# Optimization experiments

Measured on AMD Instinct MI355X. Metric: run time of the kernel, lower is better.

The kernel has to match this reference:

```python
import jax, jax.numpy as jnp
import numpy as np

B, LSEQ = 128, 4096
NUM_EXPERTS, TOP_K = 8, 2
OUT_SEQ = 256
AUX_FACTOR = 0.01


def _conv1d(x, w, b, stride, pad):
    # x: [B, Cin, L], w: [Cout, Cin, K]
    y = jax.lax.conv_general_dilated(x, w, (stride,), [(pad, pad)],
                                     dimension_numbers=('NCH', 'OIH', 'NCH'))
    return y + b[None, :, None]


def setup_inputs() -> dict:
    key = jax.random.key(0)
    ks = jax.random.split(key, 9)
    s = 0.05
    return {
        'x': jax.random.normal(ks[0], (B, LSEQ), jnp.float32),
        # gating conv net (in_channels=2 -> 32 -> 64, kernel 5, padding same)
        'g_w1': jax.random.normal(ks[1], (32, 2, 5), jnp.float32) * s,
        'g_b1': jnp.zeros((32,), jnp.float32),
        'g_w2': jax.random.normal(ks[2], (64, 32, 5), jnp.float32) * s,
        'g_b2': jnp.zeros((64,), jnp.float32),
        # gating MLP (64 -> 128 -> num_experts)
        'm_w1': jax.random.normal(ks[3], (128, 64), jnp.float32) * s,
        'm_b1': jnp.zeros((128,), jnp.float32),
        'm_w2': jax.random.normal(ks[4], (NUM_EXPERTS, 128), jnp.float32) * s,
        'm_b2': jnp.zeros((NUM_EXPERTS,), jnp.float32),
        # expert CNN stacks, stacked over experts (same shapes per expert)
        'ew1': jax.random.normal(ks[5], (NUM_EXPERTS, 64, 2, 7), jnp.float32) * s,
        'eb1': jnp.zeros((NUM_EXPERTS, 64), jnp.float32),
        'ew2': jax.random.normal(ks[6], (NUM_EXPERTS, 128, 64, 5), jnp.float32) * s,
        'eb2': jnp.zeros((NUM_EXPERTS, 128), jnp.float32),
        'ew3': jax.random.normal(ks[7], (NUM_EXPERTS, 128, 128, 3), jnp.float32) * s,
        'eb3': jnp.zeros((NUM_EXPERTS, 128), jnp.float32),
    }


def reference(x, g_w1, g_b1, g_w2, g_b2, m_w1, m_b1, m_w2, m_b2,
              ew1, eb1, ew2, eb2, ew3, eb3):
    b, lseq = x.shape
    # periodic Hann window (torch.hann_window default)
    win = 0.5 * (1.0 - jnp.cos(2.0 * jnp.pi * jnp.arange(lseq, dtype=x.dtype) / lseq))
    xf = jnp.fft.rfft(x * win, norm='ortho')
    fft = jnp.stack([xf.real, xf.imag], axis=1)  # [B, 2, Lf]

    # gating: conv -> relu -> conv -> relu -> global avg pool -> MLP (dropout in eval)
    h = jax.nn.relu(_conv1d(fft, g_w1, g_b1, 1, 2))
    h = jax.nn.relu(_conv1d(h, g_w2, g_b2, 1, 2))
    pooled = h.mean(-1)  # [B, 64]
    logits = jax.nn.relu(pooled @ m_w1.T + m_b1) @ m_w2.T + m_b2  # [B, E]
    rw = jax.nn.softmax(logits, axis=1)
    aux = AUX_FACTOR * NUM_EXPERTS * (rw.mean(0) * logits.mean(0)).sum()

    tw, ti = jax.lax.top_k(rw, TOP_K)  # [B, K]
    tw = tw / tw.sum(-1, keepdims=True)

    # Each (token, k) pair routes fft[b] to expert ti[b,k]; compute each expert
    # densely over the batch and gather (same math as masked dispatch/combine).
    def expert(w1, b1, w2, b2, w3, b3):
        e = jax.nn.relu(_conv1d(fft, w1, b1, 2, 3))
        e = jax.nn.relu(_conv1d(e, w2, b2, 2, 2))
        e = jax.nn.relu(_conv1d(e, w3, b3, 1, 1))
        return e

    out_stack = jax.vmap(expert)(ew1, eb1, ew2, eb2, ew3, eb3)  # [E, B, C, L]
    sel = out_stack[ti, jnp.arange(b)[:, None]]                 # [B, K, C, L]
    final = (sel * tw[:, :, None, None]).sum(1)                 # [B, C, L]

    # adaptive max pool 1d to OUT_SEQ (PyTorch window rule)
    L = final.shape[-1]
    starts = np.floor(np.arange(OUT_SEQ) * L / OUT_SEQ).astype(np.int32)
    ends = np.ceil((np.arange(OUT_SEQ) + 1) * L / OUT_SEQ).astype(np.int32)
    maxw = int((ends - starts).max())
    raw = starts[:, None] + np.arange(maxw)[None, :]
    valid = jnp.asarray(raw < ends[:, None])
    idx = np.minimum(raw, L - 1)
    g = final[..., idx]  # [B, C, OUT_SEQ, maxw]
    resized = jnp.max(jnp.where(valid, g, -jnp.inf), axis=-1)
    return (resized, aux)
```

## Files before the change

### kernel.cpp

```cpp
#include <hip/hip_runtime.h>

#define NFREQ 2049
#define L1LEN 1025
#define L1STRIDE 1026
#define L2LEN 513

typedef short v8s  __attribute__((ext_vector_type(8)));
typedef float v16f __attribute__((ext_vector_type(16)));
typedef unsigned short ushort_t;
typedef unsigned int uint_t;

#define OFF_FFT     0ull
#define OFF_TWID    524544ull
#define OFF_PTW     526592ull
#define OFF_WIN     530944ull
#define OFF_PART    535040ull
#define OFF_TW      1075712ull
#define OFF_TI      1075968ull
#define OFF_SRWLOG  1076224ull
#define OFF_W2HF    1076480ull
#define OFF_W2LF    1081600ull
#define OFF_W2F     1086720ull
#define OFF_W3F     1250560ull
#define OFF_A       1447168ull
#define OFF_E2U     9852160ull

#define E1U_K_STRIDE 8404992
#define E2U_K_STRIDE 8404992

__device__ __forceinline__ float relu_f(float x) { return fmaxf(x, 0.0f); }
__device__ __forceinline__ int   rfl_i(int v)   { return __builtin_amdgcn_readfirstlane(v); }
__device__ __forceinline__ float rfl_f(float v) { return __uint_as_float((unsigned)__builtin_amdgcn_readfirstlane((int)__float_as_uint(v))); }
__device__ __forceinline__ ushort_t f2bf(float x) {
    unsigned u = __float_as_uint(x);
    unsigned r = (u + 0x7FFFu + ((u >> 16) & 1u)) >> 16;
    return (ushort_t)r;
}
__device__ __forceinline__ float bf2f(ushort_t h) { return __uint_as_float(((unsigned)h) << 16); }

__global__ void init_kernel(float* SRWLOG, float* TWID, float* PTW, float* WIN,
                            ushort_t* W2HF, ushort_t* W2LF, ushort_t* W2F, ushort_t* W3F,
                            const float* g_w2, const float* ew2, const float* ew3) {
    const float PI = 3.14159265358979323846f;
    int tid = blockIdx.x * blockDim.x + threadIdx.x;
    int stride = gridDim.x * blockDim.x;
    for (int i = tid; i < 16; i += stride) SRWLOG[i] = 0.0f;
    for (int j = tid; j < 1024; j += stride) {
        float a = PI * (float)j / 1024.0f;
        TWID[2 * j] = cosf(a);
        TWID[2 * j + 1] = -sinf(a);
    }
    for (int k = tid; k < 2049; k += stride) {
        float a = PI * (float)k / 2048.0f;
        PTW[2 * k] = cosf(a);
        PTW[2 * k + 1] = sinf(a);
    }
    for (int n = tid; n < 4096; n += stride) {
        WIN[n] = 0.5f * (1.0f - cosf(2.0f * PI * (float)n / 4096.0f));
    }
    for (int i = tid; i < 10240; i += stride) {
        int j = i & 7;
        int lane = (i >> 3) & 63;
        int ks = (i >> 9) & 1;
        int tile = (i >> 10) & 1;
        int t = i >> 11;
        int o = tile * 32 + (lane & 31);
        int c = ks * 16 + (lane >> 5) * 8 + j;
        float w = g_w2[o * 160 + c * 5 + t];
        ushort_t h = f2bf(w);
        W2HF[i] = h;
        W2LF[i] = f2bf(w - bf2f(h));
    }
    for (int i = tid; i < 327680; i += stride) {
        int j = i & 7;
        int lane = (i >> 3) & 63;
        int ks = (i >> 9) & 3;
        int w = (i >> 11) & 3;
        int t = (i >> 13) % 5;
        int e = i / 40960;
        int o = w * 32 + (lane & 31);
        int c = ks * 16 + (lane >> 5) * 8 + j;
        W2F[i] = f2bf(ew2[((e * 128 + o) * 64 + c) * 5 + t]);
    }
    for (int i = tid; i < 393216; i += stride) {
        int j = i & 7;
        int lane = (i >> 3) & 63;
        int ks = (i >> 9) & 7;
        int w = (i >> 12) & 3;
        int t = (i >> 14) % 3;
        int e = i / 49152;
        int o = w * 32 + (lane & 31);
        int c = ks * 16 + (lane >> 5) * 8 + j;
        W3F[i] = f2bf(ew3[((e * 128 + o) * 128 + c) * 3 + t]);
    }
}

__global__ __launch_bounds__(1024) void fft_kernel(const float* __restrict__ x,
                                                   const float* __restrict__ TWID,
                                                   const float* __restrict__ PTW,
                                                   const float* __restrict__ WIN,
                                                   float* __restrict__ FFT) {
    __shared__ float re[2048];
    __shared__ float im[2048];
    int b = blockIdx.x, t = threadIdx.x;
    const float* xb = x + b * 4096;
    for (int i = t; i < 2048; i += 1024) {
        int j = (int)(__brev((unsigned)i) >> 21);
        re[i] = xb[2 * j] * WIN[2 * j];
        im[i] = xb[2 * j + 1] * WIN[2 * j + 1];
    }
    for (int s = 1; s <= 11; ++s) {
        __syncthreads();
        int half = 1 << (s - 1);
        int shift = 11 - s;
        int bf = t;
        {
            int grp = bf >> (s - 1);
            int pos = bf & (half - 1);
            int i1 = (grp << s) + pos;
            int i2 = i1 + half;
            int j = pos << shift;
            float wr = TWID[2 * j], wi = TWID[2 * j + 1];
            float ar = re[i2], ai = im[i2];
            float tr = wr * ar - wi * ai;
            float ti = wr * ai + wi * ar;
            float br = re[i1], bi = im[i1];
            re[i2] = br - tr; im[i2] = bi - ti;
            re[i1] = br + tr; im[i1] = bi + ti;
        }
    }
    __syncthreads();
    const float scale = 1.0f / 64.0f;
    for (int k = t; k <= 2048; k += 1024) {
        int k1 = k & 2047;
        int k2 = (2048 - k) & 2047;
        float zr = re[k1], zi = im[k1];
        float yr = re[k2], yi = im[k2];
        float Er = 0.5f * (zr + yr), Ei = 0.5f * (zi - yi);
        float Or = 0.5f * (zi + yi), Oi = 0.5f * (yr - zr);
        float c2 = PTW[2 * k], s3 = PTW[2 * k + 1];
        FFT[b * 4098 + k]        = (Er + c2 * Or + s3 * Oi) * scale;
        FFT[b * 4098 + 2049 + k] = (Ei + c2 * Oi - s3 * Or) * scale;
    }
}

__global__ __launch_bounds__(256) void g12_kernel(const float* __restrict__ FFT,
                                                  const float* __restrict__ g_w1, const float* __restrict__ g_b1,
                                                  const ushort_t* __restrict__ W2HF, const ushort_t* __restrict__ W2LF,
                                                  const float* __restrict__ g_b2,
                                                  float* __restrict__ PART) {
    __shared__ float fx[2][72];
    __shared__ float w1S[320];
    __shared__ float b1S[32];
    __shared__ __align__(16) char un[17408];
    ushort_t (*xh)[40] = (ushort_t (*)[40])un;
    ushort_t (*xl)[40] = (ushort_t (*)[40])(un + 5440);
    float (*red)[68]  = (float (*)[68])un;
    int b = blockIdx.y;
    int q0 = blockIdx.x * 64;
    int t = threadIdx.x;
    for (int i = t; i < 352; i += 256) {
        if (i < 320) w1S[i] = g_w1[i];
        else b1S[i - 320] = g_b1[i - 320];
    }
    {
        const float* fb = FFT + b * 4098;
        for (int i = t; i < 144; i += 256) {
            int ch = i / 72, u = i % 72;
            int P = q0 - 4 + u;
            fx[ch][u] = (P >= 0 && P < NFREQ) ? fb[ch * NFREQ + P] : 0.0f;
        }
    }
    __syncthreads();
    {
        int c = t & 31;
        float bias = b1S[c];
        float wr[10];
        #pragma unroll
        for (int j = 0; j < 10; ++j) wr[j] = w1S[c * 10 + j];
        for (int i = t; i < 544; i += 256) {
            int g4 = (i >> 5) << 2;
            float4 x00 = *(const float4*)&fx[0][g4];
            float4 x01 = *(const float4*)&fx[0][g4 + 4];
            float4 x10 = *(const float4*)&fx[1][g4];
            float4 x11 = *(const float4*)&fx[1][g4 + 4];
            float xa[8] = {x00.x, x00.y, x00.z, x00.w, x01.x, x01.y, x01.z, x01.w};
            float xb_[8] = {x10.x, x10.y, x10.z, x10.w, x11.x, x11.y, x11.z, x11.w};
            #pragma unroll
            for (int rr = 0; rr < 4; ++rr) {
                int row = g4 + rr;
                int pos = q0 - 2 + row;
                ushort_t h = 0, l = 0;
                if (pos >= 0 && pos < NFREQ) {
                    float a = bias;
                    #pragma unroll
                    for (int tt = 0; tt < 5; ++tt) a = fmaf(xa[rr + tt], wr[tt], a);
                    #pragma unroll
                    for (int tt = 0; tt < 5; ++tt) a = fmaf(xb_[rr + tt], wr[5 + tt], a);
                    a = relu_f(a);
                    h = f2bf(a);
                    l = f2bf(a - bf2f(h));
                }
                xh[row][c] = h;
                xl[row][c] = l;
            }
        }
    }
    __syncthreads();
    int lane = t & 63;
    int w = rfl_i(t >> 6);
    int tile = w & 1;
    int qh = w >> 1;
    int n = lane & 31;
    int kg = lane >> 5;
    v16f acc;
    #pragma unroll
    for (int i = 0; i < 16; ++i) acc[i] = 0.0f;
    #pragma unroll
    for (int t5 = 0; t5 < 5; ++t5) {
        int row = qh * 32 + n + t5;
        #pragma unroll
        for (int ks = 0; ks < 2; ++ks) {
            int c0 = ks * 16 + kg * 8;
            v8s Ah = *(const v8s*)(W2HF + (((t5 * 2 + tile) * 2 + ks) << 9) + lane * 8);
            v8s Al = *(const v8s*)(W2LF + (((t5 * 2 + tile) * 2 + ks) << 9) + lane * 8);
            v8s Bh = *(const v8s*)&xh[row][c0];
            v8s Bl = *(const v8s*)&xl[row][c0];
            acc = __builtin_amdgcn_mfma_f32_32x32x16_bf16(Ah, Bh, acc, 0, 0, 0);
            acc = __builtin_amdgcn_mfma_f32_32x32x16_bf16(Ah, Bl, acc, 0, 0, 0);
            acc = __builtin_amdgcn_mfma_f32_32x32x16_bf16(Al, Bh, acc, 0, 0, 0);
        }
    }
    __syncthreads();
    {
        int q = q0 + qh * 32 + n;
        bool valid = (q < NFREQ);
        #pragma unroll
        for (int r = 0; r < 16; ++r) {
            int m = (r & 3) + 8 * (r >> 2) + 4 * kg;
            int o = tile * 32 + m;
            red[o][qh * 32 + n] = valid ? relu_f(acc[r] + g_b2[o]) : 0.0f;
        }
    }
    __syncthreads();
    {
        int o = t >> 2;
        int qq = t & 3;
        float s = 0.0f;
        #pragma unroll
        for (int u = 0; u < 4; ++u) {
            float4 vv = *(const float4*)&red[o][qq * 16 + u * 4];
            s += vv.x + vv.y + vv.z + vv.w;
        }
        s += __shfl_xor(s, 1, 64);
        s += __shfl_xor(s, 2, 64);
        if (qq == 0) PART[(b * 64 + o) * 66 + blockIdx.x] = s;
    }
}

__global__ __launch_bounds__(128) void mlp_kernel(const float* __restrict__ PART,
                                                  const float* __restrict__ m_w1, const float* __restrict__ m_b1,
                                                  const float* __restrict__ m_w2, const float* __restrict__ m_b2,
                                                  float* TW, int* TI, float* SRWLOG) {
    __shared__ float pooledS[64];
    __shared__ float hid[128];
    __shared__ float lgS[8];
    __shared__ float rwS[8];
    int b = blockIdx.x, t = threadIdx.x;
    if (t < 64) {
        float s = 0.0f;
        const float* pp = PART + (b * 64 + t) * 66;
        for (int blk = 0; blk < 33; ++blk) s += pp[blk];
        pooledS[t] = s;
    }
    __syncthreads();
    const float inv = 1.0f / 2049.0f;
    {
        float h = m_b1[t];
        for (int c = 0; c < 64; ++c)
            h = fmaf(pooledS[c] * inv, m_w1[t * 64 + c], h);
        hid[t] = relu_f(h);
    }
    __syncthreads();
    if (t < 8) {
        float lg = m_b2[t];
        for (int j = 0; j < 128; ++j) lg = fmaf(hid[j], m_w2[t * 128 + j], lg);
        lgS[t] = lg;
    }
    __syncthreads();
    if (t == 0) {
        float mx = lgS[0];
        for (int e = 1; e < 8; ++e) mx = fmaxf(mx, lgS[e]);
        float s = 0.0f, ex[8];
        for (int e = 0; e < 8; ++e) { ex[e] = expf(lgS[e] - mx); s += ex[e]; }
        for (int e = 0; e < 8; ++e) rwS[e] = ex[e] / s;
        int i1 = 0;
        for (int e = 1; e < 8; ++e) if (rwS[e] > rwS[i1]) i1 = e;
        int i2 = (i1 == 0) ? 1 : 0;
        for (int e = 0; e < 8; ++e) if (e != i1 && rwS[e] > rwS[i2]) i2 = e;
        float t0 = rwS[i1], t1 = rwS[i2], sm = t0 + t1;
        TW[b * 2] = t0 / sm; TW[b * 2 + 1] = t1 / sm;
        TI[b * 2] = i1; TI[b * 2 + 1] = i2;
    }
    __syncthreads();
    if (t < 8) {
        atomicAdd(&SRWLOG[t], rwS[t]);
        atomicAdd(&SRWLOG[8 + t], lgS[t]);
    }
}

__global__ __launch_bounds__(256) void e1_kernel(const float* __restrict__ FFT,
                                                 const float* __restrict__ ew1, const float* __restrict__ eb1,
                                                 const int* __restrict__ TI, ushort_t* __restrict__ E1u) {
    __shared__ float xs[2][520];
    int r0 = blockIdx.x * 256;
    int b = blockIdx.y;
    int k = blockIdx.z;
    int t = threadIdx.x;
    int e = rfl_i(TI[b * 2 + k]);
    int lo = 2 * r0 - 3;
    const float* fb = FFT + b * 4098;
    for (int i = t; i < 2 * 520; i += 256) {
        int ch = i / 520, off = i % 520;
        int pos = lo + off;
        xs[ch][off] = (pos >= 0 && pos < NFREQ) ? fb[ch * NFREQ + pos] : 0.0f;
    }
    __syncthreads();
    int r = r0 + t;
    if (r >= L1LEN) return;
    float xv[14];
    #pragma unroll
    for (int ch = 0; ch < 2; ++ch)
        #pragma unroll
        for (int tt = 0; tt < 7; ++tt)
            xv[ch * 7 + tt] = xs[ch][2 * t + tt];
    const float* wb = ew1 + e * 64 * 14;
    const float* bb = eb1 + e * 64;
    ushort_t* outb = E1u + (size_t)k * E1U_K_STRIDE + (size_t)b * 64 * L1STRIDE + r;
    bool last = (r == L1LEN - 1);
    for (int o = 0; o < 64; ++o) {
        float a = bb[o];
        const float* w = wb + o * 14;
        #pragma unroll
        for (int j = 0; j < 14; ++j)
            a = fmaf(xv[j], w[j], a);
        outb[o * L1STRIDE] = f2bf(relu_f(a));
        if (last) outb[o * L1STRIDE + 1] = 0;
    }
}

__global__ __launch_bounds__(256) void e2_kernel(const ushort_t* __restrict__ E1u,
                                                 const ushort_t* __restrict__ W2F, const float* __restrict__ eb2,
                                                 const int* __restrict__ TI, ushort_t* __restrict__ E2u) {
    __shared__ __align__(16) char sm2[19008];
    ushort_t (*xe)[72] = (ushort_t (*)[72])sm2;
    ushort_t (*xo)[72] = (ushort_t (*)[72])(sm2 + 9504);
    ushort_t (*oT)[136] = (ushort_t (*)[136])sm2;
    int b = blockIdx.x;
    int k = blockIdx.z;
    int q0 = blockIdx.y * 64;
    int t = threadIdx.x;
    int e = rfl_i(TI[b * 2 + k]);
    const ushort_t* E1k = E1u + (size_t)k * E1U_K_STRIDE;
    for (int i = t; i < 64 * 66; i += 256) {
        int c = i / 66, j = i % 66;
        int p = 2 * q0 - 2 + 2 * j;
        uint_t v = 0;
        if (p >= 0 && p < L1LEN)
            v = *(const uint_t*)(E1k + (size_t)(b * 64 + c) * L1STRIDE + p);
        xe[j][c] = (ushort_t)(v & 0xFFFFu);
        xo[j][c] = (ushort_t)(v >> 16);
    }
    __syncthreads();
    int lane = t & 63;
    int w = rfl_i(t >> 6);
    int n = lane & 31;
    int kg = lane >> 5;
    v16f acc0, acc1;
    #pragma unroll
    for (int i = 0; i < 16; ++i) { acc0[i] = 0.0f; acc1[i] = 0.0f; }
    #pragma unroll
    for (int t5 = 0; t5 < 5; ++t5) {
        int roff = t5 >> 1;
        const ushort_t (*sel)[72] = (t5 & 1) ? xo : xe;
        const ushort_t* wfrag = W2F + ((((e * 5 + t5) * 4 + w) * 4) << 9) + lane * 8;
        #pragma unroll
        for (int ks = 0; ks < 4; ++ks) {
            int c0 = ks * 16 + kg * 8;
            v8s a = *(const v8s*)(wfrag + (ks << 9));
            v8s b0 = *(const v8s*)&sel[n + roff][c0];
            v8s b1 = *(const v8s*)&sel[n + 32 + roff][c0];
            acc0 = __builtin_amdgcn_mfma_f32_32x32x16_bf16(a, b0, acc0, 0, 0, 0);
            acc1 = __builtin_amdgcn_mfma_f32_32x32x16_bf16(a, b1, acc1, 0, 0, 0);
        }
    }
    __syncthreads();
    #pragma unroll
    for (int g = 0; g < 4; ++g) {
        int ob = w * 32 + 8 * g + 4 * kg;
        uint_t p00 = (uint_t)f2bf(relu_f(acc0[4 * g + 0] + eb2[e * 128 + ob + 0]))
                   | ((uint_t)f2bf(relu_f(acc0[4 * g + 1] + eb2[e * 128 + ob + 1])) << 16);
        uint_t p01 = (uint_t)f2bf(relu_f(acc0[4 * g + 2] + eb2[e * 128 + ob + 2]))
                   | ((uint_t)f2bf(relu_f(acc0[4 * g + 3] + eb2[e * 128 + ob + 3])) << 16);
        uint_t p10 = (uint_t)f2bf(relu_f(acc1[4 * g + 0] + eb2[e * 128 + ob + 0]))
                   | ((uint_t)f2bf(relu_f(acc1[4 * g + 1] + eb2[e * 128 + ob + 1])) << 16);
        uint_t p11 = (uint_t)f2bf(relu_f(acc1[4 * g + 2] + eb2[e * 128 + ob + 2]))
                   | ((uint_t)f2bf(relu_f(acc1[4 * g + 3] + eb2[e * 128 + ob + 3])) << 16);
        uint2 v0; v0.x = p00; v0.y = p01;
        uint2 v1; v1.x = p10; v1.y = p11;
        *(uint2*)&oT[n][ob]      = v0;
        *(uint2*)&oT[32 + n][ob] = v1;
    }
    __syncthreads();
    ushort_t* E2k = E2u + (size_t)k * E2U_K_STRIDE;
    for (int i = t; i < 64 * 16; i += 256) {
        int qq = i >> 4, c8 = (i & 15) * 8;
        int q = q0 + qq;
        if (q < L2LEN)
            *(uint4*)(E2k + ((size_t)b * L2LEN + q) * 128 + c8) = *(const uint4*)&oT[qq][c8];
    }
}

__global__ __launch_bounds__(256) void e3_kernel(const ushort_t* __restrict__ E2u,
                                                 const ushort_t* __restrict__ W3F, const float* __restrict__ eb3,
                                                 const int* __restrict__ TI, const float* __restrict__ TW,
                                                 float* __restrict__ FINAL) {
    __shared__ __align__(16) ushort_t xT[2][66][136];
    int b = blockIdx.x;
    int q0 = blockIdx.y * 64;
    int t = threadIdx.x;
    int lane = t & 63;
    int ow = rfl_i(t >> 6);
    int n = lane & 31;
    int kg = lane >> 5;
    int e0  = rfl_i(TI[b * 2]);
    int e1_ = rfl_i(TI[b * 2 + 1]);
    float wk0 = rfl_f(TW[b * 2]);
    float wk1 = rfl_f(TW[b * 2 + 1]);
    for (int i = t; i < 1056; i += 256) {
        int row = i >> 4, c8 = (i & 15) * 8;
        int pos = q0 - 1 + row;
        uint4 v; v.x = 0u; v.y = 0u; v.z = 0u; v.w = 0u;
        if (pos >= 0 && pos < L2LEN)
            v = *(const uint4*)(E2u + ((size_t)b * L2LEN + pos) * 128 + c8);
        *(uint4*)&xT[0][row][c8] = v;
    }
    __syncthreads();
    uint4 st[5];
    #pragma unroll
    for (int j = 0; j < 5; ++j) {
        int i = t + j * 256;
        uint4 v; v.x = 0u; v.y = 0u; v.z = 0u; v.w = 0u;
        if (i < 1056) {
            int row = i >> 4, c8 = (i & 15) * 8;
            int pos = q0 - 1 + row;
            if (pos >= 0 && pos < L2LEN)
                v = *(const uint4*)(E2u + (size_t)E2U_K_STRIDE + ((size_t)b * L2LEN + pos) * 128 + c8);
        }
        st[j] = v;
    }
    float res0[16], res1[16];
    #pragma unroll
    for (int i = 0; i < 16; ++i) { res0[i] = 0.0f; res1[i] = 0.0f; }
    {
        v16f a0, a1;
        #pragma unroll
        for (int i = 0; i < 16; ++i) { a0[i] = 0.0f; a1[i] = 0.0f; }
        #pragma unroll
        for (int t3 = 0; t3 < 3; ++t3) {
            const ushort_t* wfrag = W3F + ((((e0 * 3 + t3) * 4 + ow) * 8) << 9) + lane * 8;
            #pragma unroll
            for (int ks = 0; ks < 8; ++ks) {
                int c0 = ks * 16 + kg * 8;
                v8s a = *(const v8s*)(wfrag + (ks << 9));
                v8s b0 = *(const v8s*)&xT[0][n + t3][c0];
                v8s b1 = *(const v8s*)&xT[0][32 + n + t3][c0];
                a0 = __builtin_amdgcn_mfma_f32_32x32x16_bf16(a, b0, a0, 0, 0, 0);
                a1 = __builtin_amdgcn_mfma_f32_32x32x16_bf16(a, b1, a1, 0, 0, 0);
            }
        }
        #pragma unroll
        for (int r = 0; r < 16; ++r) {
            int m = (r & 3) + 8 * (r >> 2) + 4 * kg;
            float bias = eb3[e0 * 128 + ow * 32 + m];
            res0[r] += relu_f(a0[r] + bias) * wk0;
            res1[r] += relu_f(a1[r] + bias) * wk0;
        }
    }
    #pragma unroll
    for (int j = 0; j < 5; ++j) {
        int i = t + j * 256;
        if (i < 1056) {
            int row = i >> 4, c8 = (i & 15) * 8;
            *(uint4*)&xT[1][row][c8] = st[j];
        }
    }
    __syncthreads();
    {
        v16f a0, a1;
        #pragma unroll
        for (int i = 0; i < 16; ++i) { a0[i] = 0.0f; a1[i] = 0.0f; }
        #pragma unroll
        for (int t3 = 0; t3 < 3; ++t3) {
            const ushort_t* wfrag = W3F + ((((e1_ * 3 + t3) * 4 + ow) * 8) << 9) + lane * 8;
            #pragma unroll
            for (int ks = 0; ks < 8; ++ks) {
                int c0 = ks * 16 + kg * 8;
                v8s a = *(const v8s*)(wfrag + (ks << 9));
                v8s b0 = *(const v8s*)&xT[1][n + t3][c0];
                v8s b1 = *(const v8s*)&xT[1][32 + n + t3][c0];
                a0 = __builtin_amdgcn_mfma_f32_32x32x16_bf16(a, b0, a0, 0, 0, 0);
                a1 = __builtin_amdgcn_mfma_f32_32x32x16_bf16(a, b1, a1, 0, 0, 0);
            }
        }
        #pragma unroll
        for (int r = 0; r < 16; ++r) {
            int m = (r & 3) + 8 * (r >> 2) + 4 * kg;
            float bias = eb3[e1_ * 128 + ow * 32 + m];
            res0[r] += relu_f(a0[r] + bias) * wk1;
            res1[r] += relu_f(a1[r] + bias) * wk1;
        }
    }
    float* Fb = FINAL + (size_t)b * 128 * 513;
    int qA = q0 + n;
    int qB = q0 + 32 + n;
    #pragma unroll
    for (int r = 0; r < 16; ++r) {
        int m = (r & 3) + 8 * (r >> 2) + 4 * kg;
        int o = ow * 32 + m;
        if (qA < L2LEN) Fb[o * 513 + qA] = res0[r];
        if (qB < L2LEN) Fb[o * 513 + qB] = res1[r];
    }
}

__global__ __launch_bounds__(256) void pool_kernel(const float* __restrict__ FINAL,
                                                   const float* __restrict__ SRWLOG,
                                                   float* __restrict__ out) {
    if (blockIdx.x == 0 && threadIdx.x == 0) {
        float a = 0.0f;
        for (int e = 0; e < 8; ++e)
            a += (SRWLOG[e] / 128.0f) * (SRWLOG[8 + e] / 128.0f);
        out[4194304] = 0.01f * 8.0f * a;
    }
    int idx = blockIdx.x * 256 + threadIdx.x;
    int j = idx & 255;
    int row = idx >> 8;
    const float* f = FINAL + (size_t)row * 513;
    int s = (513 * j) >> 8;
    int e_ = (513 * (j + 1) + 255) >> 8;
    float m = f[s];
    for (int p = s + 1; p < e_; ++p) m = fmaxf(m, f[p]);
    out[idx] = m;
}

extern "C" void kernel_launch(void* const* d_in, const int* in_sizes, int n_in,
                              void* d_out, int out_size, void* d_ws, size_t ws_size,
                              hipStream_t stream) {
    const float* x    = (const float*)d_in[0];
    const float* g_w1 = (const float*)d_in[1];
    const float* g_b1 = (const float*)d_in[2];
    const float* g_w2 = (const float*)d_in[3];
    const float* g_b2 = (const float*)d_in[4];
    const float* m_w1 = (const float*)d_in[5];
    const float* m_b1 = (const float*)d_in[6];
    const float* m_w2 = (const float*)d_in[7];
    const float* m_b2 = (const float*)d_in[8];
    const float* ew1  = (const float*)d_in[9];
    const float* eb1  = (const float*)d_in[10];
    const float* ew2  = (const float*)d_in[11];
    const float* eb2  = (const float*)d_in[12];
    const float* ew3  = (const float*)d_in[13];
    const float* eb3  = (const float*)d_in[14];

    float* ws     = (float*)d_ws;
    float* FFT    = ws + OFF_FFT;
    float* TWID   = ws + OFF_TWID;
    float* PTW    = ws + OFF_PTW;
    float* WIN    = ws + OFF_WIN;
    float* PART   = ws + OFF_PART;
    float* TW     = ws + OFF_TW;
    int*   TI     = (int*)(ws + OFF_TI);
    float* SRWLOG = ws + OFF_SRWLOG;
    ushort_t* W2HF = (ushort_t*)(ws + OFF_W2HF);
    ushort_t* W2LF = (ushort_t*)(ws + OFF_W2LF);
    ushort_t* W2F  = (ushort_t*)(ws + OFF_W2F);
    ushort_t* W3F  = (ushort_t*)(ws + OFF_W3F);
    ushort_t* E1u = (ushort_t*)(ws + OFF_A);
    float* FINAL  = ws + OFF_A;
    ushort_t* E2u = (ushort_t*)(ws + OFF_E2U);
    float* out    = (float*)d_out;

    init_kernel<<<512, 256, 0, stream>>>(SRWLOG, TWID, PTW, WIN, W2HF, W2LF, W2F, W3F, g_w2, ew2, ew3);
    fft_kernel<<<128, 1024, 0, stream>>>(x, TWID, PTW, WIN, FFT);
    g12_kernel<<<dim3(33, 128), 256, 0, stream>>>(FFT, g_w1, g_b1, W2HF, W2LF, g_b2, PART);
    mlp_kernel<<<128, 128, 0, stream>>>(PART, m_w1, m_b1, m_w2, m_b2, TW, TI, SRWLOG);
    e1_kernel<<<dim3(5, 128, 2), 256, 0, stream>>>(FFT, ew1, eb1, TI, E1u);
    e2_kernel<<<dim3(128, 9, 2), 256, 0, stream>>>(E1u, W2F, eb2, TI, E2u);
    e3_kernel<<<dim3(128, 9), 256, 0, stream>>>(E2u, W3F, eb3, TI, TW, FINAL);
    pool_kernel<<<16384, 256, 0, stream>>>(FINAL, SRWLOG, out);
}
```

Measured before the change: 234.4 us.

## Fuse expert conv1 into conv2 kernel, recomputing the conv1 halo in shared memory

```diff
diff --git a/kernel.cpp b/kernel.cpp
--- a/kernel.cpp
+++ b/kernel.cpp
@@ -2,7 +2,6 @@
 
 #define NFREQ 2049
 #define L1LEN 1025
-#define L1STRIDE 1026
 #define L2LEN 513
 
 typedef short v8s  __attribute__((ext_vector_type(8)));
@@ -25,7 +24,6 @@
 #define OFF_A       1447168ull
 #define OFF_E2U     9852160ull
 
-#define E1U_K_STRIDE 8404992
 #define E2U_K_STRIDE 8404992
 
 __device__ __forceinline__ float relu_f(float x) { return fmaxf(x, 0.0f); }
@@ -309,49 +307,11 @@
     }
 }
 
-__global__ __launch_bounds__(256) void e1_kernel(const float* __restrict__ FFT,
-                                                 const float* __restrict__ ew1, const float* __restrict__ eb1,
-                                                 const int* __restrict__ TI, ushort_t* __restrict__ E1u) {
-    __shared__ float xs[2][520];
-    int r0 = blockIdx.x * 256;
-    int b = blockIdx.y;
-    int k = blockIdx.z;
-    int t = threadIdx.x;
-    int e = rfl_i(TI[b * 2 + k]);
-    int lo = 2 * r0 - 3;
-    const float* fb = FFT + b * 4098;
-    for (int i = t; i < 2 * 520; i += 256) {
-        int ch = i / 520, off = i % 520;
-        int pos = lo + off;
-        xs[ch][off] = (pos >= 0 && pos < NFREQ) ? fb[ch * NFREQ + pos] : 0.0f;
-    }
-    __syncthreads();
-    int r = r0 + t;
-    if (r >= L1LEN) return;
-    float xv[14];
-    #pragma unroll
-    for (int ch = 0; ch < 2; ++ch)
-        #pragma unroll
-        for (int tt = 0; tt < 7; ++tt)
-            xv[ch * 7 + tt] = xs[ch][2 * t + tt];
-    const float* wb = ew1 + e * 64 * 14;
-    const float* bb = eb1 + e * 64;
-    ushort_t* outb = E1u + (size_t)k * E1U_K_STRIDE + (size_t)b * 64 * L1STRIDE + r;
-    bool last = (r == L1LEN - 1);
-    for (int o = 0; o < 64; ++o) {
-        float a = bb[o];
-        const float* w = wb + o * 14;
-        #pragma unroll
-        for (int j = 0; j < 14; ++j)
-            a = fmaf(xv[j], w[j], a);
-        outb[o * L1STRIDE] = f2bf(relu_f(a));
-        if (last) outb[o * L1STRIDE + 1] = 0;
-    }
-}
-
-__global__ __launch_bounds__(256) void e2_kernel(const ushort_t* __restrict__ E1u,
-                                                 const ushort_t* __restrict__ W2F, const float* __restrict__ eb2,
-                                                 const int* __restrict__ TI, ushort_t* __restrict__ E2u) {
+__global__ __launch_bounds__(256) void e12_kernel(const float* __restrict__ FFT,
+                                                  const float* __restrict__ ew1, const float* __restrict__ eb1,
+                                                  const ushort_t* __restrict__ W2F, const float* __restrict__ eb2,
+                                                  const int* __restrict__ TI, ushort_t* __restrict__ E2u) {
+    __shared__ float fxs[2][272];
     __shared__ __align__(16) char sm2[19008];
     ushort_t (*xe)[72] = (ushort_t (*)[72])sm2;
     ushort_t (*xo)[72] = (ushort_t (*)[72])(sm2 + 9504);
@@ -361,15 +321,36 @@
     int q0 = blockIdx.y * 64;
     int t = threadIdx.x;
     int e = rfl_i(TI[b * 2 + k]);
-    const ushort_t* E1k = E1u + (size_t)k * E1U_K_STRIDE;
-    for (int i = t; i < 64 * 66; i += 256) {
-        int c = i / 66, j = i % 66;
-        int p = 2 * q0 - 2 + 2 * j;
-        uint_t v = 0;
-        if (p >= 0 && p < L1LEN)
-            v = *(const uint_t*)(E1k + (size_t)(b * 64 + c) * L1STRIDE + p);
-        xe[j][c] = (ushort_t)(v & 0xFFFFu);
-        xo[j][c] = (ushort_t)(v >> 16);
+    {
+        const float* fb = FFT + b * 4098;
+        for (int i = t; i < 544; i += 256) {
+            int ch = i / 272, off = i - ch * 272;
+            int P = 4 * q0 - 7 + off;
+            fxs[ch][off] = (P >= 0 && P < NFREQ) ? fb[ch * NFREQ + P] : 0.0f;
+        }
+    }
+    int c = t & 63;
+    float w1r[14];
+    #pragma unroll
+    for (int j = 0; j < 14; ++j) w1r[j] = ew1[(e * 64 + c) * 14 + j];
+    float b1r = eb1[e * 64 + c];
+    __syncthreads();
+    {
+        int g0 = t >> 6;
+        for (int r = g0; r < 132; r += 4) {
+            int p = 2 * q0 - 2 + r;
+            ushort_t val = 0;
+            if (p >= 0 && p < L1LEN) {
+                float a = b1r;
+                #pragma unroll
+                for (int tt = 0; tt < 7; ++tt) a = fmaf(fxs[0][2 * r + tt], w1r[tt], a);
+                #pragma unroll
+                for (int tt = 0; tt < 7; ++tt) a = fmaf(fxs[1][2 * r + tt], w1r[7 + tt], a);
+                val = f2bf(relu_f(a));
+            }
+            if (r & 1) xo[r >> 1][c] = val;
+            else       xe[r >> 1][c] = val;
+        }
     }
     __syncthreads();
     int lane = t & 63;
@@ -585,7 +566,6 @@
     ushort_t* W2LF = (ushort_t*)(ws + OFF_W2LF);
     ushort_t* W2F  = (ushort_t*)(ws + OFF_W2F);
     ushort_t* W3F  = (ushort_t*)(ws + OFF_W3F);
-    ushort_t* E1u = (ushort_t*)(ws + OFF_A);
     float* FINAL  = ws + OFF_A;
     ushort_t* E2u = (ushort_t*)(ws + OFF_E2U);
     float* out    = (float*)d_out;
@@ -594,8 +574,7 @@
     fft_kernel<<<128, 1024, 0, stream>>>(x, TWID, PTW, WIN, FFT);
     g12_kernel<<<dim3(33, 128), 256, 0, stream>>>(FFT, g_w1, g_b1, W2HF, W2LF, g_b2, PART);
     mlp_kernel<<<128, 128, 0, stream>>>(PART, m_w1, m_b1, m_w2, m_b2, TW, TI, SRWLOG);
-    e1_kernel<<<dim3(5, 128, 2), 256, 0, stream>>>(FFT, ew1, eb1, TI, E1u);
-    e2_kernel<<<dim3(128, 9, 2), 256, 0, stream>>>(E1u, W2F, eb2, TI, E2u);
+    e12_kernel<<<dim3(128, 9, 2), 256, 0, stream>>>(FFT, ew1, eb1, W2F, eb2, TI, E2u);
     e3_kernel<<<dim3(128, 9), 256, 0, stream>>>(E2u, W3F, eb3, TI, TW, FINAL);
     pool_kernel<<<16384, 256, 0, stream>>>(FINAL, SRWLOG, out);
 }
```

After: 216.9 us (median of 2 runs). 1.08x faster.
